# Kernel tuning notes

Measured on AMD Instinct MI355X. Metric: run time of the kernel, lower is better.

The kernel has to match this reference:

```python
import jax, jax.numpy as jnp
import numpy as np

N = 50000   # nodes
E = 640000  # edges
IN, H, OUT = 128, 128, 64
BN_EPS = 1e-5


def setup_inputs() -> dict:
    key = jax.random.key(0)
    ks = jax.random.split(key, 16)
    inp = {}
    inp["x"] = jax.random.normal(ks[0], (N, IN), jnp.float32)
    inp["edge_index"] = jax.random.randint(ks[1], (2, E), 0, N, dtype=jnp.int32)
    # BatchNorm affine params (nontrivial so grads are informative)
    inp["bn_in_gamma"] = 1.0 + 0.1 * jax.random.normal(ks[2], (IN,), jnp.float32)
    inp["bn_in_beta"] = 0.1 * jax.random.normal(ks[3], (IN,), jnp.float32)
    inp["bn1_gamma"] = 1.0 + 0.1 * jax.random.normal(ks[4], (H,), jnp.float32)
    inp["bn1_beta"] = 0.1 * jax.random.normal(ks[5], (H,), jnp.float32)
    inp["bn2_gamma"] = 1.0 + 0.1 * jax.random.normal(ks[6], (OUT,), jnp.float32)
    inp["bn2_beta"] = 0.1 * jax.random.normal(ks[7], (OUT,), jnp.float32)
    # Linear / GCNConv weights (fan-in scaled)
    inp["proj_W"] = jax.random.normal(ks[8], (IN, H), jnp.float32) / np.sqrt(IN)
    inp["proj_b"] = jnp.zeros((H,), jnp.float32)
    inp["conv1_W"] = jax.random.normal(ks[9], (H, H), jnp.float32) / np.sqrt(H)
    inp["conv1_b"] = jnp.zeros((H,), jnp.float32)
    inp["conv2_W"] = jax.random.normal(ks[10], (H, OUT), jnp.float32) / np.sqrt(H)
    inp["conv2_b"] = jnp.zeros((OUT,), jnp.float32)
    return inp


def batchnorm(x, gamma, beta):
    # training-mode BN: batch statistics (biased variance), per-feature affine
    m = jnp.mean(x, axis=0)
    v = jnp.mean(jnp.square(x - m), axis=0)
    return (x - m) * jax.lax.rsqrt(v + BN_EPS) * gamma + beta


def gcn_conv(x, src, dst, W, b):
    # PyG GCNConv: y = D^{-1/2} (A + I) D^{-1/2} (x W) + b
    xw = x @ W                                    # [N, F_out]
    loops = jnp.arange(N, dtype=src.dtype)
    s = jnp.concatenate([src, loops])             # [E + N]
    d = jnp.concatenate([dst, loops])
    deg = jax.ops.segment_sum(jnp.ones_like(d, jnp.float32), d, num_segments=N)
    dinv = jnp.where(deg > 0, jax.lax.rsqrt(deg), 0.0)
    norm = dinv[s] * dinv[d]                      # [E + N]
    msgs = xw[s] * norm[:, None]                  # gather + per-edge scale
    out = jax.ops.segment_sum(msgs, d, num_segments=N)  # scatter-add
    return out + b


def reference(x, edge_index, bn_in_gamma, bn_in_beta, bn1_gamma, bn1_beta,
              bn2_gamma, bn2_beta, proj_W, proj_b, conv1_W, conv1_b,
              conv2_W, conv2_b):
    src, dst = edge_index[0], edge_index[1]
    h = batchnorm(x, bn_in_gamma, bn_in_beta)
    h = jax.nn.relu(h @ proj_W + proj_b)
    h = jax.nn.relu(batchnorm(gcn_conv(h, src, dst, conv1_W, conv1_b),
                              bn1_gamma, bn1_beta))
    # dropout: identity in eval mode
    out = batchnorm(gcn_conv(h, src, dst, conv2_W, conv2_b),
                    bn2_gamma, bn2_beta)
    return out
```

## Files before the change

### kernel.cpp

```cpp
#include <hip/hip_runtime.h>

#define NN 50000
#define NE 640000
#define BNEPS 1e-5f
#define NBANK 16
#define CAP 64

#define OFF_DINV 0
#define OFF_CURSOR 51200
#define OFF_ESRC 102400
#define OFF_WT0 3302400
#define OFF_WT1 3310592
#define OFF_WT2 3318784
#define OFF_STATS 3322880
#define OFF_B0 3333120
#define OFF_B1 9733120

typedef __attribute__((ext_vector_type(8))) __bf16 bf16x8;
typedef __attribute__((ext_vector_type(4))) float f32x4;

__device__ __forceinline__ float uplo(unsigned int u) {
  unsigned int v = u << 16;
  return __builtin_bit_cast(float, v);
}
__device__ __forceinline__ float uphi(unsigned int u) {
  unsigned int v = u & 0xffff0000u;
  return __builtin_bit_cast(float, v);
}
__device__ __forceinline__ unsigned int f2bf(float f) {
  unsigned int u = __builtin_bit_cast(unsigned int, f);
  return (u + 0x7fffu + ((u >> 16) & 1u)) >> 16;
}

__global__ __launch_bounds__(256) void prep_k(
    const float* __restrict__ W0, const float* __restrict__ W1,
    const float* __restrict__ W2, unsigned short* __restrict__ T0,
    unsigned short* __restrict__ T1, unsigned short* __restrict__ T2,
    int* __restrict__ cursor, float* __restrict__ stats) {
  const int bid = blockIdx.x;
  const int tid = threadIdx.x;
  if (bid < 160) {
    int f = bid * 256 + tid;
    if (f < 16384) {
      int k = f >> 7, n = f & 127;
      T0[n * 128 + k] = (unsigned short)f2bf(W0[f]);
    } else if (f < 32768) {
      int g = f - 16384;
      int k = g >> 7, n = g & 127;
      T1[n * 128 + k] = (unsigned short)f2bf(W1[g]);
    } else if (f < 40960) {
      int g = f - 32768;
      int k = g >> 6, n = g & 63;
      T2[n * 128 + k] = (unsigned short)f2bf(W2[g]);
    }
  } else if (bid < 356) {
    int i = (bid - 160) * 256 + tid;
    if (i < NN) cursor[i] = i * CAP;
  } else {
    int j = (bid - 356) * 256 + tid;
    stats[j] = 0.0f;
  }
}

template <int NC, int MODE>
__device__ __forceinline__ void bn_stats_body(
    int sbid, int nsb, int tid, const float* __restrict__ A,
    const float* __restrict__ dinv, const float* __restrict__ cb,
    float* __restrict__ sums, float* __restrict__ sqs,
    float (*rs)[NC], float (*rq)[NC]) {
  constexpr int CG = NC / 4;
  constexpr int RG = 256 / CG;
  const int tc = tid % CG;
  const int tr = tid / CG;
  float cb0 = 0, cb1 = 0, cb2 = 0, cb3 = 0;
  if (MODE == 1) {
    cb0 = cb[tc * 4];
    cb1 = cb[tc * 4 + 1];
    cb2 = cb[tc * 4 + 2];
    cb3 = cb[tc * 4 + 3];
  }
  float s0 = 0, s1 = 0, s2 = 0, s3 = 0, q0 = 0, q1 = 0, q2 = 0, q3 = 0;
  const int stride = nsb * RG;
  for (int r = sbid * RG + tr; r < NN; r += stride) {
    float4 v = *(const float4*)&A[(size_t)r * NC + tc * 4];
    if (MODE == 1) {
      float di = dinv[r];
      v.x = fmaf(v.x, di, cb0);
      v.y = fmaf(v.y, di, cb1);
      v.z = fmaf(v.z, di, cb2);
      v.w = fmaf(v.w, di, cb3);
    }
    s0 += v.x; s1 += v.y; s2 += v.z; s3 += v.w;
    q0 += v.x * v.x; q1 += v.y * v.y; q2 += v.z * v.z; q3 += v.w * v.w;
  }
  rs[tr][tc * 4] = s0; rs[tr][tc * 4 + 1] = s1;
  rs[tr][tc * 4 + 2] = s2; rs[tr][tc * 4 + 3] = s3;
  rq[tr][tc * 4] = q0; rq[tr][tc * 4 + 1] = q1;
  rq[tr][tc * 4 + 2] = q2; rq[tr][tc * 4 + 3] = q3;
  __syncthreads();
  if (tr == 0) {
    const int bank = (sbid & (NBANK - 1)) * NC;
    for (int j = 0; j < 4; ++j) {
      int c = tc * 4 + j;
      float ts = 0, tq = 0;
      for (int g = 0; g < RG; ++g) { ts += rs[g][c]; tq += rq[g][c]; }
      atomicAdd(&sums[bank + c], ts);
      atomicAdd(&sqs[bank + c], tq);
    }
  }
}

__global__ __launch_bounds__(256) void stats_fill_k(
    const float* __restrict__ x, float* __restrict__ s0,
    float* __restrict__ q0, const int* __restrict__ src,
    const int* __restrict__ dst, int* __restrict__ cursor,
    int* __restrict__ esrc) {
  __shared__ float rs[8][128];
  __shared__ float rq[8][128];
  const int bid = blockIdx.x;
  if (bid < 1024) {
    bn_stats_body<128, 0>(bid, 1024, threadIdx.x, x, nullptr, nullptr, s0, q0,
                          rs, rq);
  } else {
    int e = (bid - 1024) * 256 + threadIdx.x;
    if (e < NE) {
      int p = atomicAdd(&cursor[dst[e]], 1);
      esrc[p] = src[e];
    }
  }
}

template <int NC, int PRE, int EPI>
__device__ __forceinline__ void gemm_body(
    int bid, int tid, char* __restrict__ smem, float* __restrict__ af_s,
    float* __restrict__ bf_s, const void* __restrict__ Ain,
    const unsigned short* __restrict__ Wt, const float* __restrict__ bias,
    const float* __restrict__ sums, const float* __restrict__ sqs,
    const float* __restrict__ gamma, const float* __restrict__ beta,
    const float* __restrict__ preb, const float* __restrict__ dinv,
    unsigned short* __restrict__ O1) {
  constexpr int TM = 64;
  constexpr int NTILES = NC / 16;
  constexpr int CSTR = NC + 4;
  const int row0 = bid * TM;

  if constexpr (PRE != 1) {
    if (tid < 128) {
      float s = 0.f, q = 0.f;
#pragma unroll
      for (int b = 0; b < NBANK; ++b) {
        s += sums[b * 128 + tid];
        q += sqs[b * 128 + tid];
      }
      float m = s * (1.0f / NN);
      float v = q * (1.0f / NN) - m * m;
      float a = gamma[tid] * rsqrtf(v + BNEPS);
      af_s[tid] = a;
      bf_s[tid] = beta[tid] - m * a;
    }
    __syncthreads();
    const float* A = (const float*)Ain;
    for (int f = tid; f < TM * 32; f += 256) {
      const int r = f >> 5;
      const int c4 = f & 31;
      const int rg = row0 + r;
      float4 v = make_float4(0.f, 0.f, 0.f, 0.f);
      if (rg < NN) {
        v = *(const float4*)&A[(size_t)rg * 128 + c4 * 4];
        const float4 a4 = *(const float4*)&af_s[c4 * 4];
        const float4 b4 = *(const float4*)&bf_s[c4 * 4];
        if (PRE == 0) {
          v.x = fmaf(a4.x, v.x, b4.x);
          v.y = fmaf(a4.y, v.y, b4.y);
          v.z = fmaf(a4.z, v.z, b4.z);
          v.w = fmaf(a4.w, v.w, b4.w);
        } else {
          const float di = dinv[rg];
          const float4 p4 = *(const float4*)&preb[c4 * 4];
          v.x = fmaxf(fmaf(a4.x, fmaf(di, v.x, p4.x), b4.x), 0.f);
          v.y = fmaxf(fmaf(a4.y, fmaf(di, v.y, p4.y), b4.y), 0.f);
          v.z = fmaxf(fmaf(a4.z, fmaf(di, v.z, p4.z), b4.z), 0.f);
          v.w = fmaxf(fmaf(a4.w, fmaf(di, v.w, p4.w), b4.w), 0.f);
        }
      }
      uint2 wv;
      wv.x = f2bf(v.x) | (f2bf(v.y) << 16);
      wv.y = f2bf(v.z) | (f2bf(v.w) << 16);
      const int ba = (r * 256 + c4 * 8) ^ ((r & 7) << 4);
      *(uint2*)(smem + ba) = wv;
    }
    __syncthreads();
  }

  const int w = tid >> 6;
  const int l = tid & 63;
  const int lr = l & 15;
  const int lg = l >> 4;
  f32x4 acc[NTILES];
#pragma unroll
  for (int i = 0; i < NTILES; ++i) acc[i] = (f32x4){0.f, 0.f, 0.f, 0.f};
  const int arow = w * 16 + lr;
#pragma unroll
  for (int kt = 0; kt < 4; ++kt) {
    bf16x8 a;
    if constexpr (PRE == 1) {
      const unsigned short* Ab = (const unsigned short*)Ain;
      a = __builtin_bit_cast(
          bf16x8,
          *(const uint4*)&Ab[(size_t)(row0 + arow) * 128 + kt * 32 + lg * 8]);
    } else {
      const int ba = (arow * 256 + kt * 64 + lg * 16) ^ ((arow & 7) << 4);
      a = __builtin_bit_cast(bf16x8, *(const uint4*)(smem + ba));
    }
#pragma unroll
    for (int nt = 0; nt < NTILES; ++nt) {
      bf16x8 b = __builtin_bit_cast(
          bf16x8,
          *(const uint4*)&Wt[(size_t)(nt * 16 + lr) * 128 + kt * 32 + lg * 8]);
      acc[nt] = __builtin_amdgcn_mfma_f32_16x16x32_bf16(a, b, acc[nt], 0, 0, 0);
    }
  }
  __syncthreads();

  float* Cl = (float*)smem;
#pragma unroll
  for (int nt = 0; nt < NTILES; ++nt)
#pragma unroll
    for (int r = 0; r < 4; ++r)
      Cl[(w * 16 + lg * 4 + r) * CSTR + nt * 16 + lr] = acc[nt][r];
  __syncthreads();

  constexpr int CG = NC / 4;
  constexpr int RPT = TM * CG / 256;
  const int tc = tid % CG;
  const int tr = tid / CG;
  float4 b4 = make_float4(0.f, 0.f, 0.f, 0.f);
  if constexpr (EPI == 0) b4 = *(const float4*)&bias[tc * 4];
#pragma unroll
  for (int i = 0; i < RPT; ++i) {
    const int row = tr * RPT + i;
    const int rg = row0 + row;
    if (rg < NN) {
      float4 v = *(const float4*)&Cl[row * CSTR + tc * 4];
      if (EPI == 0) {
        v.x = fmaxf(v.x + b4.x, 0.f);
        v.y = fmaxf(v.y + b4.y, 0.f);
        v.z = fmaxf(v.z + b4.z, 0.f);
        v.w = fmaxf(v.w + b4.w, 0.f);
      }
      uint2 o;
      o.x = f2bf(v.x) | (f2bf(v.y) << 16);
      o.y = f2bf(v.z) | (f2bf(v.w) << 16);
      *(uint2*)&O1[(size_t)rg * NC + tc * 4] = o;
    }
  }
}

__global__ __launch_bounds__(256) void gemm1_dinv_k(
    const float* __restrict__ x, const unsigned short* __restrict__ Wt0,
    const float* __restrict__ proj_b, const float* __restrict__ s0,
    const float* __restrict__ q0, const float* __restrict__ g0,
    const float* __restrict__ b0, unsigned short* __restrict__ H1bf,
    const int* __restrict__ cursor, float* __restrict__ dinv) {
  __shared__ __align__(16) char smem[33792];
  __shared__ float af_s[128];
  __shared__ float bf_s[128];
  const int bid = blockIdx.x;
  const int tid = threadIdx.x;
  if (bid < 782) {
    gemm_body<128, 0, 0>(bid, tid, smem, af_s, bf_s, x, Wt0, proj_b, s0, q0,
                         g0, b0, nullptr, nullptr, H1bf);
  } else {
    int i = (bid - 782) * 256 + tid;
    if (i < NN) {
      int d = cursor[i] - i * CAP;
      dinv[i] = rsqrtf((float)d + 1.0f);
    }
  }
}

template <int NC>
__global__ __launch_bounds__(256) void gather_bf_k(
    const int* __restrict__ cursor, const int* __restrict__ esrc,
    const unsigned short* __restrict__ Y, const float* __restrict__ dinv,
    float* __restrict__ ACC) {
  constexpr int CG = NC / 8;
  constexpr int RG = 256 / CG;
  const int tc = threadIdx.x % CG;
  const int tr = threadIdx.x / CG;
  const int n = blockIdx.x * RG + tr;
  if (n >= NN) return;
  const int c = tc * 8;
  float a[8];
  {
    const float dn = dinv[n];
    const uint4 p = *(const uint4*)&Y[(size_t)n * NC + c];
    a[0] = dn * uplo(p.x); a[1] = dn * uphi(p.x);
    a[2] = dn * uplo(p.y); a[3] = dn * uphi(p.y);
    a[4] = dn * uplo(p.z); a[5] = dn * uphi(p.z);
    a[6] = dn * uplo(p.w); a[7] = dn * uphi(p.w);
  }
  const int beg = n * CAP;
  const int end = cursor[n];
  int e = beg;
  for (; e + 2 <= end; e += 2) {
    const int s0 = esrc[e];
    const int s1 = esrc[e + 1];
    const float d0 = dinv[s0];
    const float d1 = dinv[s1];
    const uint4 q0 = *(const uint4*)&Y[(size_t)s0 * NC + c];
    const uint4 q1 = *(const uint4*)&Y[(size_t)s1 * NC + c];
    a[0] = fmaf(d0, uplo(q0.x), a[0]); a[1] = fmaf(d0, uphi(q0.x), a[1]);
    a[2] = fmaf(d0, uplo(q0.y), a[2]); a[3] = fmaf(d0, uphi(q0.y), a[3]);
    a[4] = fmaf(d0, uplo(q0.z), a[4]); a[5] = fmaf(d0, uphi(q0.z), a[5]);
    a[6] = fmaf(d0, uplo(q0.w), a[6]); a[7] = fmaf(d0, uphi(q0.w), a[7]);
    a[0] = fmaf(d1, uplo(q1.x), a[0]); a[1] = fmaf(d1, uphi(q1.x), a[1]);
    a[2] = fmaf(d1, uplo(q1.y), a[2]); a[3] = fmaf(d1, uphi(q1.y), a[3]);
    a[4] = fmaf(d1, uplo(q1.z), a[4]); a[5] = fmaf(d1, uphi(q1.z), a[5]);
    a[6] = fmaf(d1, uplo(q1.w), a[6]); a[7] = fmaf(d1, uphi(q1.w), a[7]);
  }
  if (e < end) {
    const int s0 = esrc[e];
    const float d0 = dinv[s0];
    const uint4 q0 = *(const uint4*)&Y[(size_t)s0 * NC + c];
    a[0] = fmaf(d0, uplo(q0.x), a[0]); a[1] = fmaf(d0, uphi(q0.x), a[1]);
    a[2] = fmaf(d0, uplo(q0.y), a[2]); a[3] = fmaf(d0, uphi(q0.y), a[3]);
    a[4] = fmaf(d0, uplo(q0.z), a[4]); a[5] = fmaf(d0, uphi(q0.z), a[5]);
    a[6] = fmaf(d0, uplo(q0.w), a[6]); a[7] = fmaf(d0, uphi(q0.w), a[7]);
  }
  *(float4*)&ACC[(size_t)n * NC + c] = make_float4(a[0], a[1], a[2], a[3]);
  *(float4*)&ACC[(size_t)n * NC + c + 4] = make_float4(a[4], a[5], a[6], a[7]);
}

template <int NC, int MODE>
__global__ __launch_bounds__(256) void bn_stats_k(const float* __restrict__ A,
                                                  const float* __restrict__ dinv,
                                                  const float* __restrict__ cb,
                                                  float* __restrict__ sums,
                                                  float* __restrict__ sqs) {
  __shared__ float rs[256 / (NC / 4)][NC];
  __shared__ float rq[256 / (NC / 4)][NC];
  bn_stats_body<NC, MODE>(blockIdx.x, gridDim.x, threadIdx.x, A, dinv, cb,
                          sums, sqs, rs, rq);
}

template <int NC, int PRE, int EPI>
__global__ __launch_bounds__(256) void mfma_gemm_k(
    const void* __restrict__ Ain, const unsigned short* __restrict__ Wt,
    const float* __restrict__ bias, const float* __restrict__ sums,
    const float* __restrict__ sqs, const float* __restrict__ gamma,
    const float* __restrict__ beta, const float* __restrict__ preb,
    const float* __restrict__ dinv, unsigned short* __restrict__ O1) {
  constexpr int CBYTES = 64 * (NC + 4) * 4;
  constexpr int SMEM = (CBYTES > 16384) ? CBYTES : 16384;
  __shared__ __align__(16) char smem[SMEM];
  __shared__ float af_s[128];
  __shared__ float bf_s[128];
  gemm_body<NC, PRE, EPI>(blockIdx.x, threadIdx.x, smem, af_s, bf_s, Ain, Wt,
                          bias, sums, sqs, gamma, beta, preb, dinv, O1);
}

__global__ __launch_bounds__(256) void final_k(
    const float* __restrict__ ACC2, const float* __restrict__ dinv,
    const float* __restrict__ cb, const float* __restrict__ s2,
    const float* __restrict__ q2, const float* __restrict__ gamma,
    const float* __restrict__ beta, float* __restrict__ out) {
  __shared__ float af_s[64];
  __shared__ float bf_s[64];
  if (threadIdx.x < 64) {
    float s = 0.f, q = 0.f;
#pragma unroll
    for (int b = 0; b < NBANK; ++b) {
      s += s2[b * 64 + threadIdx.x];
      q += q2[b * 64 + threadIdx.x];
    }
    float m = s * (1.0f / NN);
    float v = q * (1.0f / NN) - m * m;
    float a = gamma[threadIdx.x] * rsqrtf(v + BNEPS);
    af_s[threadIdx.x] = a;
    bf_s[threadIdx.x] = beta[threadIdx.x] - m * a;
  }
  __syncthreads();
  const int u = blockIdx.x * 256 + threadIdx.x;
  if (u >= NN * 16) return;
  const int r = u >> 4;
  const int c = (u & 15) * 4;
  const float di = dinv[r];
  float4 v = *(const float4*)&ACC2[(size_t)r * 64 + c];
  const float4 c4 = *(const float4*)&cb[c];
  const float4 a4 = *(const float4*)&af_s[c];
  const float4 b4 = *(const float4*)&bf_s[c];
  float4 o;
  o.x = fmaf(a4.x, fmaf(v.x, di, c4.x), b4.x);
  o.y = fmaf(a4.y, fmaf(v.y, di, c4.y), b4.y);
  o.z = fmaf(a4.z, fmaf(v.z, di, c4.z), b4.z);
  o.w = fmaf(a4.w, fmaf(v.w, di, c4.w), b4.w);
  *(float4*)&out[(size_t)r * 64 + c] = o;
}

extern "C" void kernel_launch(void* const* d_in, const int* in_sizes, int n_in,
                              void* d_out, int out_size, void* d_ws,
                              size_t ws_size, hipStream_t stream) {
  const float* x = (const float*)d_in[0];
  const int* ei = (const int*)d_in[1];
  const int* src = ei;
  const int* dst = ei + NE;
  const float* bn_in_g = (const float*)d_in[2];
  const float* bn_in_b = (const float*)d_in[3];
  const float* bn1_g = (const float*)d_in[4];
  const float* bn1_b = (const float*)d_in[5];
  const float* bn2_g = (const float*)d_in[6];
  const float* bn2_b = (const float*)d_in[7];
  const float* proj_W = (const float*)d_in[8];
  const float* proj_b = (const float*)d_in[9];
  const float* conv1_W = (const float*)d_in[10];
  const float* conv1_b = (const float*)d_in[11];
  const float* conv2_W = (const float*)d_in[12];
  const float* conv2_b = (const float*)d_in[13];
  float* out = (float*)d_out;

  float* ws = (float*)d_ws;
  float* dinv = ws + OFF_DINV;
  int* cursor = (int*)(ws + OFF_CURSOR);
  int* esrc = (int*)(ws + OFF_ESRC);
  unsigned short* Wt0 = (unsigned short*)(ws + OFF_WT0);
  unsigned short* Wt1 = (unsigned short*)(ws + OFF_WT1);
  unsigned short* Wt2 = (unsigned short*)(ws + OFF_WT2);
  float* st = ws + OFF_STATS;
  float* s0 = st;
  float* q0 = st + 2048;
  float* s1 = st + 4096;
  float* q1 = st + 6144;
  float* s2 = st + 8192;
  float* q2 = st + 9216;
  float* B0 = ws + OFF_B0;
  float* B1 = ws + OFF_B1;
  unsigned short* H1bf = (unsigned short*)B0;
  unsigned short* Ybf = (unsigned short*)B1;
  float* ACC = B0;
  unsigned short* Y2bf = (unsigned short*)B1;
  float* ACC2 = B0;

  prep_k<<<396, 256, 0, stream>>>(proj_W, conv1_W, conv2_W, Wt0, Wt1, Wt2,
                                  cursor, st);
  stats_fill_k<<<3524, 256, 0, stream>>>(x, s0, q0, src, dst, cursor, esrc);
  gemm1_dinv_k<<<978, 256, 0, stream>>>(x, Wt0, proj_b, s0, q0, bn_in_g,
                                        bn_in_b, H1bf, cursor, dinv);
  mfma_gemm_k<128, 1, 2><<<782, 256, 0, stream>>>(
      H1bf, Wt1, nullptr, nullptr, nullptr, nullptr, nullptr, nullptr, nullptr,
      Ybf);
  gather_bf_k<128><<<(NN + 15) / 16, 256, 0, stream>>>(cursor, esrc, Ybf, dinv,
                                                       ACC);
  bn_stats_k<128, 1><<<1024, 256, 0, stream>>>(ACC, dinv, conv1_b, s1, q1);
  mfma_gemm_k<64, 2, 2><<<782, 256, 0, stream>>>(
      ACC, Wt2, nullptr, s1, q1, bn1_g, bn1_b, conv1_b, dinv, Y2bf);
  gather_bf_k<64><<<(NN + 31) / 32, 256, 0, stream>>>(cursor, esrc, Y2bf, dinv,
                                                      ACC2);
  bn_stats_k<64, 1><<<1024, 256, 0, stream>>>(ACC2, dinv, conv2_b, s2, q2);
  final_k<<<(NN * 16 + 255) / 256, 256, 0, stream>>>(ACC2, dinv, conv2_b, s2,
                                                     q2, bn2_g, bn2_b, out);
}
```

Baseline: 185.9 us.

## Store edge sources as uint16 and re-pair edge fill with GEMM kernels

Edge source indices in the CSR bucket array are now stored as 16-bit values, halving the esrc footprint that the gather kernels read. The edge bucketing fill moves from the input-stats kernel into the first GEMM launch, and the dinv computation is merged with the conv1 GEMM, so the launch count stays the same. The schedule is rebalanced so stats run alone and the atomic fill overlaps the first GEMM. Truncating to uint16 is wrong because node ids reach 49999, which exceeds 65535? No, 49999 fits in uint16, so it is safe for N=50000, but it hardcodes the assumption that N stays at or below 65536.

```diff
diff --git a/kernel.cpp b/kernel.cpp
--- a/kernel.cpp
+++ b/kernel.cpp
@@ -9,12 +9,12 @@
 #define OFF_DINV 0
 #define OFF_CURSOR 51200
 #define OFF_ESRC 102400
-#define OFF_WT0 3302400
-#define OFF_WT1 3310592
-#define OFF_WT2 3318784
-#define OFF_STATS 3322880
-#define OFF_B0 3333120
-#define OFF_B1 9733120
+#define OFF_WT0 1702400
+#define OFF_WT1 1710592
+#define OFF_WT2 1718784
+#define OFF_STATS 1726976
+#define OFF_B0 1737216
+#define OFF_B1 8137216
 
 typedef __attribute__((ext_vector_type(8))) __bf16 bf16x8;
 typedef __attribute__((ext_vector_type(4))) float f32x4;
@@ -110,24 +110,16 @@
   }
 }
 
-__global__ __launch_bounds__(256) void stats_fill_k(
-    const float* __restrict__ x, float* __restrict__ s0,
-    float* __restrict__ q0, const int* __restrict__ src,
-    const int* __restrict__ dst, int* __restrict__ cursor,
-    int* __restrict__ esrc) {
-  __shared__ float rs[8][128];
-  __shared__ float rq[8][128];
-  const int bid = blockIdx.x;
-  if (bid < 1024) {
-    bn_stats_body<128, 0>(bid, 1024, threadIdx.x, x, nullptr, nullptr, s0, q0,
-                          rs, rq);
-  } else {
-    int e = (bid - 1024) * 256 + threadIdx.x;
-    if (e < NE) {
-      int p = atomicAdd(&cursor[dst[e]], 1);
-      esrc[p] = src[e];
-    }
-  }
+template <int NC, int MODE>
+__global__ __launch_bounds__(256) void bn_stats_k(const float* __restrict__ A,
+                                                  const float* __restrict__ dinv,
+                                                  const float* __restrict__ cb,
+                                                  float* __restrict__ sums,
+                                                  float* __restrict__ sqs) {
+  __shared__ float rs[256 / (NC / 4)][NC];
+  __shared__ float rq[256 / (NC / 4)][NC];
+  bn_stats_body<NC, MODE>(blockIdx.x, gridDim.x, threadIdx.x, A, dinv, cb,
+                          sums, sqs, rs, rq);
 }
 
 template <int NC, int PRE, int EPI>
@@ -256,12 +248,13 @@
   }
 }
 
-__global__ __launch_bounds__(256) void gemm1_dinv_k(
+__global__ __launch_bounds__(256) void gemm1_fill_k(
     const float* __restrict__ x, const unsigned short* __restrict__ Wt0,
     const float* __restrict__ proj_b, const float* __restrict__ s0,
     const float* __restrict__ q0, const float* __restrict__ g0,
     const float* __restrict__ b0, unsigned short* __restrict__ H1bf,
-    const int* __restrict__ cursor, float* __restrict__ dinv) {
+    const int* __restrict__ src, const int* __restrict__ dst,
+    int* __restrict__ cursor, unsigned short* __restrict__ esrc) {
   __shared__ __align__(16) char smem[33792];
   __shared__ float af_s[128];
   __shared__ float bf_s[128];
@@ -271,6 +264,28 @@
     gemm_body<128, 0, 0>(bid, tid, smem, af_s, bf_s, x, Wt0, proj_b, s0, q0,
                          g0, b0, nullptr, nullptr, H1bf);
   } else {
+    int e = (bid - 782) * 256 + tid;
+    if (e < NE) {
+      int p = atomicAdd(&cursor[dst[e]], 1);
+      esrc[p] = (unsigned short)src[e];
+    }
+  }
+}
+
+__global__ __launch_bounds__(256) void conv1_dinv_k(
+    const unsigned short* __restrict__ H1bf,
+    const unsigned short* __restrict__ Wt1, unsigned short* __restrict__ Ybf,
+    const int* __restrict__ cursor, float* __restrict__ dinv) {
+  __shared__ __align__(16) char smem[33792];
+  __shared__ float af_s[128];
+  __shared__ float bf_s[128];
+  const int bid = blockIdx.x;
+  const int tid = threadIdx.x;
+  if (bid < 782) {
+    gemm_body<128, 1, 2>(bid, tid, smem, af_s, bf_s, H1bf, Wt1, nullptr,
+                         nullptr, nullptr, nullptr, nullptr, nullptr, nullptr,
+                         Ybf);
+  } else {
     int i = (bid - 782) * 256 + tid;
     if (i < NN) {
       int d = cursor[i] - i * CAP;
@@ -281,7 +296,7 @@
 
 template <int NC>
 __global__ __launch_bounds__(256) void gather_bf_k(
-    const int* __restrict__ cursor, const int* __restrict__ esrc,
+    const int* __restrict__ cursor, const unsigned short* __restrict__ esrc,
     const unsigned short* __restrict__ Y, const float* __restrict__ dinv,
     float* __restrict__ ACC) {
   constexpr int CG = NC / 8;
@@ -330,18 +345,6 @@
   }
   *(float4*)&ACC[(size_t)n * NC + c] = make_float4(a[0], a[1], a[2], a[3]);
   *(float4*)&ACC[(size_t)n * NC + c + 4] = make_float4(a[4], a[5], a[6], a[7]);
-}
-
-template <int NC, int MODE>
-__global__ __launch_bounds__(256) void bn_stats_k(const float* __restrict__ A,
-                                                  const float* __restrict__ dinv,
-                                                  const float* __restrict__ cb,
-                                                  float* __restrict__ sums,
-                                                  float* __restrict__ sqs) {
-  __shared__ float rs[256 / (NC / 4)][NC];
-  __shared__ float rq[256 / (NC / 4)][NC];
-  bn_stats_body<NC, MODE>(blockIdx.x, gridDim.x, threadIdx.x, A, dinv, cb,
-                          sums, sqs, rs, rq);
 }
 
 template <int NC, int PRE, int EPI>
@@ -422,7 +425,7 @@
   float* ws = (float*)d_ws;
   float* dinv = ws + OFF_DINV;
   int* cursor = (int*)(ws + OFF_CURSOR);
-  int* esrc = (int*)(ws + OFF_ESRC);
+  unsigned short* esrc = (unsigned short*)(ws + OFF_ESRC);
   unsigned short* Wt0 = (unsigned short*)(ws + OFF_WT0);
   unsigned short* Wt1 = (unsigned short*)(ws + OFF_WT1);
   unsigned short* Wt2 = (unsigned short*)(ws + OFF_WT2);
@@ -443,12 +446,10 @@
 
   prep_k<<<396, 256, 0, stream>>>(proj_W, conv1_W, conv2_W, Wt0, Wt1, Wt2,
                                   cursor, st);
-  stats_fill_k<<<3524, 256, 0, stream>>>(x, s0, q0, src, dst, cursor, esrc);
-  gemm1_dinv_k<<<978, 256, 0, stream>>>(x, Wt0, proj_b, s0, q0, bn_in_g,
-                                        bn_in_b, H1bf, cursor, dinv);
-  mfma_gemm_k<128, 1, 2><<<782, 256, 0, stream>>>(
-      H1bf, Wt1, nullptr, nullptr, nullptr, nullptr, nullptr, nullptr, nullptr,
-      Ybf);
+  bn_stats_k<128, 0><<<1024, 256, 0, stream>>>(x, nullptr, nullptr, s0, q0);
+  gemm1_fill_k<<<3282, 256, 0, stream>>>(x, Wt0, proj_b, s0, q0, bn_in_g,
+                                         bn_in_b, H1bf, src, dst, cursor, esrc);
+  conv1_dinv_k<<<978, 256, 0, stream>>>(H1bf, Wt1, Ybf, cursor, dinv);
   gather_bf_k<128><<<(NN + 15) / 16, 256, 0, stream>>>(cursor, esrc, Ybf, dinv,
                                                        ACC);
   bn_stats_k<128, 1><<<1024, 256, 0, stream>>>(ACC, dinv, conv1_b, s1, q1);
```

Measured after the change: 177.8 us. -4.3%, faster.
